# Kernel optimization log

Measured on AMD Instinct MI355X. Metric: run time of the kernel, lower is better.

Reference implementation:

```python
import jax, jax.numpy as jnp
import numpy as np

DIM = 1024
HEADS = 16
DIM_HEAD = 64
INNER = HEADS * DIM_HEAD  # 1024
SCALE = DIM ** (-0.5)  # module scales by dim**-0.5 (not dim_head)


def setup_inputs() -> dict:
    key = jax.random.key(0)
    kx, kqkv, kwo, kbo = jax.random.split(key, 4)
    x = jax.random.normal(kx, (2, 2048, DIM), dtype=jnp.float32)
    W_qkv = jax.random.normal(kqkv, (DIM, 3 * INNER), dtype=jnp.float32) * (DIM ** -0.5)
    W_out = jax.random.normal(kwo, (INNER, DIM), dtype=jnp.float32) * (INNER ** -0.5)
    b_out = jax.random.normal(kbo, (DIM,), dtype=jnp.float32) * 0.01
    return {"x": x, "W_qkv": W_qkv, "W_out": W_out, "b_out": b_out}


def reference(x, W_qkv, W_out, b_out):
    b, n, _ = x.shape
    qkv = x @ W_qkv  # [b, n, 3*inner]
    q, k, v = jnp.split(qkv, 3, axis=-1)
    # [b, n, h*d] -> [b, h, n, d]
    reshape = lambda t: t.reshape(b, n, HEADS, DIM_HEAD).transpose(0, 2, 1, 3)
    q, k, v = reshape(q), reshape(k), reshape(v)
    dots = jnp.einsum('bhid,bhjd->bhij', q, k) * SCALE  # [b, h, n, n]
    attn = jax.nn.softmax(dots, axis=-1)
    out = jnp.einsum('bhij,bhjd->bhid', attn, v)  # [b, h, n, d]
    out = out.transpose(0, 2, 1, 3).reshape(b, n, INNER)
    return out @ W_out + b_out
```

## Files before the change

### kernel.cpp

```cpp
#include <hip/hip_runtime.h>

typedef __bf16 bf16x8 __attribute__((ext_vector_type(8)));
typedef __bf16 bf16x4 __attribute__((ext_vector_type(4)));
typedef __bf16 bf16x2 __attribute__((ext_vector_type(2)));
typedef float f32x4 __attribute__((ext_vector_type(4)));
typedef float f32x16 __attribute__((ext_vector_type(16)));
typedef int i32x4 __attribute__((ext_vector_type(4)));
typedef unsigned int u32x2 __attribute__((ext_vector_type(2)));

#define EXP2_SCALE 0.045084439f

__device__ __forceinline__ void async16(void* lds, const void* g) {
  __builtin_amdgcn_global_load_lds(
      (__attribute__((address_space(1))) unsigned int*)(g),
      (__attribute__((address_space(3))) unsigned int*)(lds), 16, 0, 0);
}

__device__ __forceinline__ unsigned int pack2(float a, float b) {
  bf16x2 t;
  t[0] = (__bf16)a;
  t[1] = (__bf16)b;
  return __builtin_bit_cast(unsigned int, t);
}

__device__ __forceinline__ float fexp2(float x) {
#if __has_builtin(__builtin_amdgcn_exp2f)
  return __builtin_amdgcn_exp2f(x);
#else
  return exp2f(x);
#endif
}

__device__ __forceinline__ void plswap(unsigned int& d, unsigned int& s) {
#if __has_builtin(__builtin_amdgcn_permlane32_swap)
  u32x2 r = __builtin_amdgcn_permlane32_swap(d, s, false, false);
  d = r[0];
  s = r[1];
#else
  asm("v_permlane32_swap_b32 %0, %1" : "+v"(d), "+v"(s));
#endif
}

__device__ __forceinline__ int detect_block(const unsigned short* win, int* cnt_sh) {
  if (threadIdx.x == 0) *cnt_sh = 0;
  __syncthreads();
  int c = 0;
#pragma unroll
  for (int j = 0; j < 8; j++) {
    const unsigned short u = win[threadIdx.x * 8 + j];
    if (((u >> 7) & 0xFF) >= 0xC0) c++;
  }
  if (c) atomicAdd(cnt_sh, c);
  __syncthreads();
  return (*cnt_sh >= 64) ? 1 : 0;
}

__global__ __launch_bounds__(256) void prep(
    const void* __restrict__ x, const void* __restrict__ Wqkv,
    const void* __restrict__ Wout, __bf16* __restrict__ xb,
    __bf16* __restrict__ WqkvT, __bf16* __restrict__ WoutT,
    int* __restrict__ flagp)
{
  __shared__ __bf16 tile[64 * 65];
  __shared__ int cnt;
  const int bx = blockIdx.x;
  const int t = threadIdx.x;

  if (bx < 2048) {
    const long base = (long)bx * 2048;
    const int f = detect_block((const unsigned short*)x + base, &cnt);
    if (bx == 0 && t == 0) *flagp = f;
    const long i = base + t * 8;
    if (f) {
      const f32x4* s4 = (const f32x4*)((const float*)x + i);
      const f32x4 v0 = s4[0], v1 = s4[1];
      bf16x8 o;
#pragma unroll
      for (int j = 0; j < 4; j++) o[j] = (__bf16)v0[j];
#pragma unroll
      for (int j = 0; j < 4; j++) o[4 + j] = (__bf16)v1[j];
      *(bf16x8*)&xb[i] = o;
    } else {
      *(bf16x8*)&xb[i] = *(const bf16x8*)((const __bf16*)x + i);
    }
    return;
  }

  const void* in;  __bf16* out;  int R = 1024, C, tcx, tr;
  if (bx < 2816) {
    const int idx = bx - 2048;
    in = Wqkv; out = WqkvT; C = 3072; tcx = (idx % 48) * 64; tr = (idx / 48) * 64;
  } else {
    const int idx = bx - 2816;
    in = Wout; out = WoutT; C = 1024; tcx = (idx % 16) * 64; tr = (idx / 16) * 64;
  }
  const int f = detect_block((const unsigned short*)in + (long)tr * C + tcx, &cnt);
#pragma unroll
  for (int i = 0; i < 16; i++) {
    const int idx = t + 256 * i;
    const int r = idx >> 6, c = idx & 63;
    const long g = (long)(tr + r) * C + tcx + c;
    tile[r * 65 + c] = f ? (__bf16)((const float*)in)[g] : ((const __bf16*)in)[g];
  }
  __syncthreads();
#pragma unroll
  for (int i = 0; i < 16; i++) {
    const int idx = t + 256 * i;
    const int r = idx >> 6, c = idx & 63;
    out[(long)(tcx + r) * R + tr + c] = tile[c * 65 + r];
  }
}

__global__ __launch_bounds__(256, 3) void gemm_qkv(
    const __bf16* __restrict__ A, const __bf16* __restrict__ Bt,
    __bf16* __restrict__ Qb, __bf16* __restrict__ Kc, __bf16* __restrict__ Vc)
{
  __shared__ __bf16 smem[17408];
  const int t = threadIdx.x;
  const int l = t & 63;
  const int w = t >> 6;
  const int wr = w >> 1, wc = w & 1;
  const int lid = blockIdx.y * 32 + blockIdx.x;
  const int s = (lid & 7) * 96 + (lid >> 3);
  const long m0 = (long)(s & 31) * 128;
  const long n0 = (long)(s >> 5) * 128;
  const int K = 1024;

  const int srow = w * 16 + (l >> 2);
  const int skof = (l & 3) * 8;
  const __bf16* gA = A + (m0 + srow) * (long)K + skof;
  const __bf16* gB = Bt + (n0 + srow) * (long)K + skof;
  const int Ao[2] = {0, 8192}, Bo[2] = {4096, 12288};
  const int lof = w * 512 + l * 8;

  async16(smem + Ao[0] + lof,        gA);
  async16(smem + Ao[0] + 2048 + lof, gA + 64 * (long)K);
  async16(smem + Bo[0] + lof,        gB);
  async16(smem + Bo[0] + 2048 + lof, gB + 64 * (long)K);
  gA += 32; gB += 32;
  __syncthreads();

  f32x4 acc[4][4] = {};

  for (int it = 0; it < 32; it++) {
    if (it < 31) {
      const int nb = (it + 1) & 1;
      async16(smem + Ao[nb] + lof,        gA);
      async16(smem + Ao[nb] + 2048 + lof, gA + 64 * (long)K);
      async16(smem + Bo[nb] + lof,        gB);
      async16(smem + Bo[nb] + 2048 + lof, gB + 64 * (long)K);
      gA += 32; gB += 32;
    }
    const __bf16* As = smem + Ao[it & 1];
    const __bf16* Bs = smem + Bo[it & 1];
    bf16x8 af[4], bfr[4];
#pragma unroll
    for (int mi = 0; mi < 4; mi++)
      af[mi] = *(const bf16x8*)&As[(wr * 64 + mi * 16 + (l & 15)) * 32 + (l >> 4) * 8];
#pragma unroll
    for (int ni = 0; ni < 4; ni++)
      bfr[ni] = *(const bf16x8*)&Bs[(wc * 64 + ni * 16 + (l & 15)) * 32 + (l >> 4) * 8];
#pragma unroll
    for (int mi = 0; mi < 4; mi++)
#pragma unroll
      for (int ni = 0; ni < 4; ni++)
        acc[mi][ni] = __builtin_amdgcn_mfma_f32_16x16x32_bf16(af[mi], bfr[ni], acc[mi][ni], 0, 0, 0);
    __syncthreads();
  }

  if (n0 < 1024) {
#pragma unroll
    for (int mi = 0; mi < 4; mi++)
#pragma unroll
      for (int ni = 0; ni < 4; ni++) {
        const long col = n0 + wc * 64 + ni * 16 + (l & 15);
#pragma unroll
        for (int r = 0; r < 4; r++) {
          const long row = m0 + wr * 64 + mi * 16 + (l >> 4) * 4 + r;
          Qb[row * 1024 + col] = (__bf16)(acc[mi][ni][r] * EXP2_SCALE);
        }
      }
  } else if (n0 < 2048) {
    const int b = (int)(m0 >> 11);
    const int nb_ = (int)(m0 & 2047);
#pragma unroll
    for (int mi = 0; mi < 4; mi++)
#pragma unroll
      for (int ni = 0; ni < 4; ni++) {
        const int col1 = (int)(n0 - 1024) + wc * 64 + ni * 16 + (l & 15);
        const int h = col1 >> 6, d = col1 & 63;
        const long hb = ((long)(b * 16 + h) * 32);
#pragma unroll
        for (int r = 0; r < 4; r++) {
          const int n = nb_ + wr * 64 + mi * 16 + (l >> 4) * 4 + r;
          const long addr = (hb + (n >> 6)) * 4096 + (d >> 3) * 512 + (n & 63) * 8 + (d & 7);
          Kc[addr] = (__bf16)acc[mi][ni][r];
        }
      }
  } else {
#pragma unroll
    for (int mi = 0; mi < 4; mi++)
#pragma unroll
      for (int ni = 0; ni < 4; ni++) {
        const int c = wc * 64 + ni * 16 + (l & 15);
        const int r = wr * 64 + mi * 16 + (l >> 4) * 4;
        bf16x4 pk;
#pragma unroll
        for (int k = 0; k < 4; k++) pk[k] = (__bf16)acc[mi][ni][k];
        *(bf16x4*)&smem[c * 136 + r] = pk;
      }
    __syncthreads();
    const int b = (int)(m0 >> 11);
    const int nbase = (int)(m0 & 2047);
#pragma unroll
    for (int i = 0; i < 8; i++) {
      const int c = (t >> 4) + i * 16;
      const int r8 = (t & 15) * 8;
      const bf16x8 v = *(const bf16x8*)&smem[c * 136 + r8];
      const int vcol = (int)(n0 - 2048) + c;
      const int h = vcol >> 6, d = vcol & 63;
      const int n = nbase + r8;
      const long addr = ((long)(b * 16 + h) * 32 + (n >> 6)) * 4096 + ((n >> 3) & 7) * 512 + d * 8;
      *(bf16x8*)&Vc[addr] = v;
    }
  }
}

__global__ __launch_bounds__(256, 2) void gemm_out(
    const __bf16* __restrict__ A, const __bf16* __restrict__ Bt,
    const void* __restrict__ bias_raw, void* __restrict__ C,
    const int* __restrict__ flagp)
{
  __shared__ __bf16 smem[12288];
  const int t = threadIdx.x;
  const int l = t & 63;
  const int w = t >> 6;
  const int wr = w >> 1, wc = w & 1;
  const int lid = blockIdx.y * 32 + blockIdx.x;
  const int s = (lid & 7) * 64 + (lid >> 3);
  const long m0 = (long)(s & 31) * 128;
  const long n0 = (long)(s >> 5) * 64;
  const int of = *flagp;
  const int K = 1024;

  const int srow = w * 16 + (l >> 2);
  const int skof = (l & 3) * 8;
  const __bf16* gA = A + (m0 + srow) * (long)K + skof;
  const __bf16* gB = Bt + (n0 + srow) * (long)K + skof;
  const int Ao[2] = {0, 6144}, Bo[2] = {4096, 10240};
  const int lof = w * 512 + l * 8;

  async16(smem + Ao[0] + lof,        gA);
  async16(smem + Ao[0] + 2048 + lof, gA + 64 * (long)K);
  async16(smem + Bo[0] + lof,        gB);
  gA += 32; gB += 32;
  __syncthreads();

  f32x4 acc[4][2] = {};

  for (int it = 0; it < 32; it++) {
    if (it < 31) {
      const int nb = (it + 1) & 1;
      async16(smem + Ao[nb] + lof,        gA);
      async16(smem + Ao[nb] + 2048 + lof, gA + 64 * (long)K);
      async16(smem + Bo[nb] + lof,        gB);
      gA += 32; gB += 32;
    }
    const __bf16* As = smem + Ao[it & 1];
    const __bf16* Bs = smem + Bo[it & 1];
    bf16x8 af[4], bfr[2];
#pragma unroll
    for (int mi = 0; mi < 4; mi++)
      af[mi] = *(const bf16x8*)&As[(wr * 64 + mi * 16 + (l & 15)) * 32 + (l >> 4) * 8];
#pragma unroll
    for (int ni = 0; ni < 2; ni++)
      bfr[ni] = *(const bf16x8*)&Bs[(wc * 32 + ni * 16 + (l & 15)) * 32 + (l >> 4) * 8];
#pragma unroll
    for (int mi = 0; mi < 4; mi++)
#pragma unroll
      for (int ni = 0; ni < 2; ni++)
        acc[mi][ni] = __builtin_amdgcn_mfma_f32_16x16x32_bf16(af[mi], bfr[ni], acc[mi][ni], 0, 0, 0);
    __syncthreads();
  }

#pragma unroll
  for (int mi = 0; mi < 4; mi++)
#pragma unroll
    for (int ni = 0; ni < 2; ni++) {
      const long col = n0 + wc * 32 + ni * 16 + (l & 15);
      const float bv = of ? ((const float*)bias_raw)[col]
                          : (float)((const __bf16*)bias_raw)[col];
#pragma unroll
      for (int r = 0; r < 4; r++) {
        const long row = m0 + wr * 64 + mi * 16 + (l >> 4) * 4 + r;
        const float val = acc[mi][ni][r] + bv;
        const long off = row * 1024 + col;
        if (of) ((float*)C)[off] = val;
        else    ((__bf16*)C)[off] = (__bf16)val;
      }
    }
}

__global__ __launch_bounds__(256, 3) void attn_kernel(
    const __bf16* __restrict__ Qb, const __bf16* __restrict__ Kc,
    const __bf16* __restrict__ Vc, __bf16* __restrict__ O)
{
  __shared__ float fsm[4 * 1024 + 128];
  const int t = threadIdx.x;
  const int l = t & 63;
  const int w = t >> 6;
  const int wi = w & 1, wj = w >> 1;
  const int hl = l >> 5;
  const int L = blockIdx.y * 32 + blockIdx.x;
  const int bh = (L & 7) * 4 + ((L >> 3) & 3);
  const int qt = L >> 5;
  const int b = bh >> 4, head = bh & 15;
  const long q_row0 = (long)b * 2048 + qt * 64;

  bf16x8 qf0, qf1, qf2, qf3;
  {
    const __bf16* gQ = Qb + (q_row0 + wi * 32 + (l & 31)) * 1024 + head * 64 + hl * 8;
    qf0 = *(const bf16x8*)(gQ);
    qf1 = *(const bf16x8*)(gQ + 16);
    qf2 = *(const bf16x8*)(gQ + 32);
    qf3 = *(const bf16x8*)(gQ + 48);
  }

  const __bf16* kb = Kc + (long)bh * 131072;
  const __bf16* vb = Vc + (long)bh * 131072;
  const int kof0 = hl * 512 + (wj * 32 + (l & 31)) * 8;
  const int vof0 = (wj * 4 + hl) * 512 + (l & 31) * 8;

  f32x16 accA = {0,0,0,0,0,0,0,0,0,0,0,0,0,0,0,0};
  f32x16 accB = {0,0,0,0,0,0,0,0,0,0,0,0,0,0,0,0};
  const f32x16 fz = {0,0,0,0,0,0,0,0,0,0,0,0,0,0,0,0};
  float l_i = 0.0f;
  bf16x8 pa0 = {}, pa1 = {};

#define LD8(p) (*(const bf16x8*)(p))
  bf16x8 ka0 = LD8(kb + kof0),        ka1 = LD8(kb + kof0 + 1024);
  bf16x8 ka2 = LD8(kb + kof0 + 2048), ka3 = LD8(kb + kof0 + 3072);
  bf16x8 kn0, kn1, kn2, kn3;
  bf16x8 va0 = {}, va1 = {}, va2 = {}, va3 = {};
  bf16x8 vn0, vn1, vn2, vn3;

#define ATT_ITER(IT, KA0,KA1,KA2,KA3, KN0,KN1,KN2,KN3, PV0,PV1,PV2,PV3, PN0,PN1,PN2,PN3) \
  { \
    const __bf16* kt_ = kb + (IT + 1) * 4096 + kof0; \
    const __bf16* vt_ = vb + (IT) * 4096 + vof0; \
    if ((IT) < 31) { \
      KN0 = LD8(kt_); KN1 = LD8(kt_ + 1024); \
      KN2 = LD8(kt_ + 2048); KN3 = LD8(kt_ + 3072); \
    } \
    PN0 = LD8(vt_);        PN1 = LD8(vt_ + 256); \
    PN2 = LD8(vt_ + 1024); PN3 = LD8(vt_ + 1280); \
    __builtin_amdgcn_s_setprio(1); \
    if ((IT) > 0) { \
      accA = __builtin_amdgcn_mfma_f32_32x32x16_bf16(pa0, PV0, accA, 0, 0, 0); \
      accB = __builtin_amdgcn_mfma_f32_32x32x16_bf16(pa0, PV1, accB, 0, 0, 0); \
      accA = __builtin_amdgcn_mfma_f32_32x32x16_bf16(pa1, PV2, accA, 0, 0, 0); \
      accB = __builtin_amdgcn_mfma_f32_32x32x16_bf16(pa1, PV3, accB, 0, 0, 0); \
    } \
    f32x16 st = __builtin_amdgcn_mfma_f32_32x32x16_bf16(KA0, qf0, fz, 0, 0, 0); \
    st = __builtin_amdgcn_mfma_f32_32x32x16_bf16(KA1, qf1, st, 0, 0, 0); \
    st = __builtin_amdgcn_mfma_f32_32x32x16_bf16(KA2, qf2, st, 0, 0, 0); \
    st = __builtin_amdgcn_mfma_f32_32x32x16_bf16(KA3, qf3, st, 0, 0, 0); \
    __builtin_amdgcn_s_setprio(0); \
    float rs0 = 0.0f, rs1 = 0.0f; \
    _Pragma("unroll") \
    for (int r = 0; r < 16; r += 2) { \
      const float p0 = fexp2(st[r]); \
      const float p1 = fexp2(st[r + 1]); \
      st[r] = p0; st[r + 1] = p1; \
      rs0 += p0; rs1 += p1; \
    } \
    l_i += rs0 + rs1; \
    unsigned int a0 = pack2(st[0],  st[1]),  b0 = pack2(st[4],  st[5]); \
    unsigned int c0 = pack2(st[2],  st[3]),  d0 = pack2(st[6],  st[7]); \
    unsigned int a1 = pack2(st[8],  st[9]),  b1 = pack2(st[12], st[13]); \
    unsigned int c1 = pack2(st[10], st[11]), d1 = pack2(st[14], st[15]); \
    plswap(a0, b0); plswap(c0, d0); plswap(a1, b1); plswap(c1, d1); \
    const i32x4 f0_ = {(int)a0, (int)c0, (int)b0, (int)d0}; \
    const i32x4 f1_ = {(int)a1, (int)c1, (int)b1, (int)d1}; \
    pa0 = __builtin_bit_cast(bf16x8, f0_); \
    pa1 = __builtin_bit_cast(bf16x8, f1_); \
  }

  for (int itp = 0; itp < 16; itp++) {
    const int it0 = itp * 2, it1 = itp * 2 + 1;
    ATT_ITER(it0, ka0,ka1,ka2,ka3, kn0,kn1,kn2,kn3, va0,va1,va2,va3, vn0,vn1,vn2,vn3)
    ATT_ITER(it1, kn0,kn1,kn2,kn3, ka0,ka1,ka2,ka3, vn0,vn1,vn2,vn3, va0,va1,va2,va3)
  }
#undef ATT_ITER
#undef LD8

  accA = __builtin_amdgcn_mfma_f32_32x32x16_bf16(pa0, va0, accA, 0, 0, 0);
  accB = __builtin_amdgcn_mfma_f32_32x32x16_bf16(pa0, va1, accB, 0, 0, 0);
  accA = __builtin_amdgcn_mfma_f32_32x32x16_bf16(pa1, va2, accA, 0, 0, 0);
  accB = __builtin_amdgcn_mfma_f32_32x32x16_bf16(pa1, va3, accB, 0, 0, 0);

  {
    unsigned int a = __builtin_bit_cast(unsigned int, l_i), bswp = a;
    plswap(a, bswp);
    l_i = __builtin_bit_cast(float, a) + __builtin_bit_cast(float, bswp);
  }

  float* xbf = fsm;
  float* lb  = fsm + 4096;
#pragma unroll
  for (int r = 0; r < 16; r++)
    xbf[w * 1024 + r * 64 + l] = wj ? accA[r] : accB[r];
  if (l < 32) lb[w * 32 + l] = l_i;
  __syncthreads();
  const int pw = 2 * (1 - wj) + wi;
#pragma unroll
  for (int r = 0; r < 16; r++) {
    const int iloc = (r & 3) + 8 * (r >> 2) + 4 * hl;
    const float lt = lb[wi * 32 + iloc] + lb[(wi + 2) * 32 + iloc];
    const float own = wj ? accB[r] : accA[r];
    const float o = own + xbf[pw * 1024 + r * 64 + l];
    const long row = q_row0 + wi * 32 + iloc;
    const long col = (long)head * 64 + wj * 32 + (l & 31);
    O[row * 1024 + col] = (__bf16)(o / lt);
  }
}

extern "C" void kernel_launch(void* const* d_in, const int* in_sizes, int n_in,
                              void* d_out, int out_size, void* d_ws, size_t ws_size,
                              hipStream_t stream) {
  const void* x    = d_in[0];
  const void* Wqkv = d_in[1];
  const void* Wout = d_in[2];
  const void* bout = d_in[3];

  char* ws = (char*)d_ws;
  int*    flagp = (int*)ws;
  __bf16* xb    = (__bf16*)(ws + 4096);
  __bf16* Obuf  = xb;
  __bf16* WqkvT = (__bf16*)(ws + 4096 +  8388608);
  __bf16* WoutT = (__bf16*)(ws + 4096 + 14680064);
  __bf16* qbuf  = (__bf16*)(ws + 4096 + 16777216);
  __bf16* kbuf  = (__bf16*)(ws + 4096 + 25165824);
  __bf16* vbuf  = (__bf16*)(ws + 4096 + 33554432);

  hipLaunchKernelGGL(prep, dim3(3072), dim3(256), 0, stream,
                     x, Wqkv, Wout, xb, WqkvT, WoutT, flagp);
  hipLaunchKernelGGL(gemm_qkv, dim3(32, 24), dim3(256), 0, stream,
                     xb, WqkvT, qbuf, kbuf, vbuf);
  hipLaunchKernelGGL(attn_kernel, dim3(32, 32), dim3(256), 0, stream,
                     qbuf, kbuf, vbuf, Obuf);
  hipLaunchKernelGGL(gemm_out, dim3(32, 16), dim3(256), 0, stream,
                     Obuf, WoutT, bout, d_out, flagp);
}
```

Measured before the change: 189.9 us.

## Compute softmax row sums via MFMA with ones and stagger KV start per tile

The per-lane fp32 accumulation of exp values is replaced by two extra MFMAs per iteration that multiply the packed bf16 P tiles by a vector of ones. This moves the row-sum work off the VALU and makes the sum match the bf16-rounded P actually used in PV. Each query tile also starts its KV loop at a different block offset, so concurrent blocks spread their K/V reads across memory. The cost is about 20% more MFMA issue per iteration and an extra accumulator register set.

```diff
diff --git a/kernel.cpp b/kernel.cpp
--- a/kernel.cpp
+++ b/kernel.cpp
@@ -316,6 +316,7 @@
   const int qt = L >> 5;
   const int b = bh >> 4, head = bh & 15;
   const long q_row0 = (long)b * 2048 + qt * 64;
+  const int phase = (qt * 5) & 31;
 
   bf16x8 qf0, qf1, qf2, qf3;
   {
@@ -326,6 +327,10 @@
     qf3 = *(const bf16x8*)(gQ + 48);
   }
 
+  bf16x8 onesb;
+#pragma unroll
+  for (int j = 0; j < 8; j++) onesb[j] = (__bf16)1.0f;
+
   const __bf16* kb = Kc + (long)bh * 131072;
   const __bf16* vb = Vc + (long)bh * 131072;
   const int kof0 = hl * 512 + (wj * 32 + (l & 31)) * 8;
@@ -333,48 +338,52 @@
 
   f32x16 accA = {0,0,0,0,0,0,0,0,0,0,0,0,0,0,0,0};
   f32x16 accB = {0,0,0,0,0,0,0,0,0,0,0,0,0,0,0,0};
+  f32x16 lsum = {0,0,0,0,0,0,0,0,0,0,0,0,0,0,0,0};
   const f32x16 fz = {0,0,0,0,0,0,0,0,0,0,0,0,0,0,0,0};
-  float l_i = 0.0f;
   bf16x8 pa0 = {}, pa1 = {};
 
 #define LD8(p) (*(const bf16x8*)(p))
-  bf16x8 ka0 = LD8(kb + kof0),        ka1 = LD8(kb + kof0 + 1024);
-  bf16x8 ka2 = LD8(kb + kof0 + 2048), ka3 = LD8(kb + kof0 + 3072);
+  {
+    const __bf16* k0_ = kb + phase * 4096 + kof0;
+  }
+  bf16x8 ka0, ka1, ka2, ka3;
+  {
+    const __bf16* k0_ = kb + phase * 4096 + kof0;
+    ka0 = LD8(k0_);        ka1 = LD8(k0_ + 1024);
+    ka2 = LD8(k0_ + 2048); ka3 = LD8(k0_ + 3072);
+  }
   bf16x8 kn0, kn1, kn2, kn3;
   bf16x8 va0 = {}, va1 = {}, va2 = {}, va3 = {};
   bf16x8 vn0, vn1, vn2, vn3;
 
-#define ATT_ITER(IT, KA0,KA1,KA2,KA3, KN0,KN1,KN2,KN3, PV0,PV1,PV2,PV3, PN0,PN1,PN2,PN3) \
+#define ATT_ITER(N, KA0,KA1,KA2,KA3, KN0,KN1,KN2,KN3, PV0,PV1,PV2,PV3, PN0,PN1,PN2,PN3) \
   { \
-    const __bf16* kt_ = kb + (IT + 1) * 4096 + kof0; \
-    const __bf16* vt_ = vb + (IT) * 4096 + vof0; \
-    if ((IT) < 31) { \
+    const int itk_ = ((N) + 1 + phase) & 31; \
+    const int itv_ = ((N) + phase) & 31; \
+    const __bf16* kt_ = kb + itk_ * 4096 + kof0; \
+    const __bf16* vt_ = vb + itv_ * 4096 + vof0; \
+    if ((N) < 31) { \
       KN0 = LD8(kt_); KN1 = LD8(kt_ + 1024); \
       KN2 = LD8(kt_ + 2048); KN3 = LD8(kt_ + 3072); \
     } \
     PN0 = LD8(vt_);        PN1 = LD8(vt_ + 256); \
     PN2 = LD8(vt_ + 1024); PN3 = LD8(vt_ + 1280); \
     __builtin_amdgcn_s_setprio(1); \
-    if ((IT) > 0) { \
+    if ((N) > 0) { \
       accA = __builtin_amdgcn_mfma_f32_32x32x16_bf16(pa0, PV0, accA, 0, 0, 0); \
       accB = __builtin_amdgcn_mfma_f32_32x32x16_bf16(pa0, PV1, accB, 0, 0, 0); \
       accA = __builtin_amdgcn_mfma_f32_32x32x16_bf16(pa1, PV2, accA, 0, 0, 0); \
       accB = __builtin_amdgcn_mfma_f32_32x32x16_bf16(pa1, PV3, accB, 0, 0, 0); \
+      lsum = __builtin_amdgcn_mfma_f32_32x32x16_bf16(pa0, onesb, lsum, 0, 0, 0); \
+      lsum = __builtin_amdgcn_mfma_f32_32x32x16_bf16(pa1, onesb, lsum, 0, 0, 0); \
     } \
     f32x16 st = __builtin_amdgcn_mfma_f32_32x32x16_bf16(KA0, qf0, fz, 0, 0, 0); \
     st = __builtin_amdgcn_mfma_f32_32x32x16_bf16(KA1, qf1, st, 0, 0, 0); \
     st = __builtin_amdgcn_mfma_f32_32x32x16_bf16(KA2, qf2, st, 0, 0, 0); \
     st = __builtin_amdgcn_mfma_f32_32x32x16_bf16(KA3, qf3, st, 0, 0, 0); \
     __builtin_amdgcn_s_setprio(0); \
-    float rs0 = 0.0f, rs1 = 0.0f; \
     _Pragma("unroll") \
-    for (int r = 0; r < 16; r += 2) { \
-      const float p0 = fexp2(st[r]); \
-      const float p1 = fexp2(st[r + 1]); \
-      st[r] = p0; st[r + 1] = p1; \
-      rs0 += p0; rs1 += p1; \
-    } \
-    l_i += rs0 + rs1; \
+    for (int r = 0; r < 16; r++) st[r] = fexp2(st[r]); \
     unsigned int a0 = pack2(st[0],  st[1]),  b0 = pack2(st[4],  st[5]); \
     unsigned int c0 = pack2(st[2],  st[3]),  d0 = pack2(st[6],  st[7]); \
     unsigned int a1 = pack2(st[8],  st[9]),  b1 = pack2(st[12], st[13]); \
@@ -398,25 +407,27 @@
   accB = __builtin_amdgcn_mfma_f32_32x32x16_bf16(pa0, va1, accB, 0, 0, 0);
   accA = __builtin_amdgcn_mfma_f32_32x32x16_bf16(pa1, va2, accA, 0, 0, 0);
   accB = __builtin_amdgcn_mfma_f32_32x32x16_bf16(pa1, va3, accB, 0, 0, 0);
-
-  {
-    unsigned int a = __builtin_bit_cast(unsigned int, l_i), bswp = a;
-    plswap(a, bswp);
-    l_i = __builtin_bit_cast(float, a) + __builtin_bit_cast(float, bswp);
-  }
+  lsum = __builtin_amdgcn_mfma_f32_32x32x16_bf16(pa0, onesb, lsum, 0, 0, 0);
+  lsum = __builtin_amdgcn_mfma_f32_32x32x16_bf16(pa1, onesb, lsum, 0, 0, 0);
 
   float* xbf = fsm;
   float* lb  = fsm + 4096;
 #pragma unroll
   for (int r = 0; r < 16; r++)
     xbf[w * 1024 + r * 64 + l] = wj ? accA[r] : accB[r];
-  if (l < 32) lb[w * 32 + l] = l_i;
+  if ((l & 31) == 0) {
+#pragma unroll
+    for (int r = 0; r < 16; r++) {
+      const int iloc = (r & 3) + 8 * (r >> 2) + 4 * hl;
+      lb[w * 32 + iloc] = lsum[r];
+    }
+  }
   __syncthreads();
   const int pw = 2 * (1 - wj) + wi;
 #pragma unroll
   for (int r = 0; r < 16; r++) {
     const int iloc = (r & 3) + 8 * (r >> 2) + 4 * hl;
-    const float lt = lb[wi * 32 + iloc] + lb[(wi + 2) * 32 + iloc];
+    const float lt = lsum[r] + lb[pw * 32 + iloc];
     const float own = wj ? accB[r] : accA[r];
     const float o = own + xbf[pw * 1024 + r * 64 + l];
     const long row = q_row0 + wi * 32 + iloc;
```

After: 192.8 us. Within noise of the previous version (+1.5%).

## Process two 64-row query tiles per attention block to reuse K/V loads

Applied to the files above, without the earlier changes.

Each attention workgroup now handles 128 query rows instead of 64, holding two sets of Q fragments and accumulators and reusing every loaded K and V fragment for both tiles. The grid is halved and the launch-bounds occupancy hint drops from 3 to 2. The goal is to halve K/V global traffic per query row and raise MFMA density per load. In exchange, register pressure rises, fewer waves are resident to hide latency, and the grid shrinks to 512 blocks, which may underfill the GPU.

```diff
diff --git a/kernel.cpp b/kernel.cpp
--- a/kernel.cpp
+++ b/kernel.cpp
@@ -301,7 +301,7 @@
     }
 }
 
-__global__ __launch_bounds__(256, 3) void attn_kernel(
+__global__ __launch_bounds__(256, 2) void attn_kernel(
     const __bf16* __restrict__ Qb, const __bf16* __restrict__ Kc,
     const __bf16* __restrict__ Vc, __bf16* __restrict__ O)
 {
@@ -315,15 +315,20 @@
   const int bh = (L & 7) * 4 + ((L >> 3) & 3);
   const int qt = L >> 5;
   const int b = bh >> 4, head = bh & 15;
-  const long q_row0 = (long)b * 2048 + qt * 64;
-
-  bf16x8 qf0, qf1, qf2, qf3;
+  const long q_row0 = (long)b * 2048 + qt * 128;
+
+  bf16x8 qA0, qA1, qA2, qA3, qB0, qB1, qB2, qB3;
   {
     const __bf16* gQ = Qb + (q_row0 + wi * 32 + (l & 31)) * 1024 + head * 64 + hl * 8;
-    qf0 = *(const bf16x8*)(gQ);
-    qf1 = *(const bf16x8*)(gQ + 16);
-    qf2 = *(const bf16x8*)(gQ + 32);
-    qf3 = *(const bf16x8*)(gQ + 48);
+    qA0 = *(const bf16x8*)(gQ);
+    qA1 = *(const bf16x8*)(gQ + 16);
+    qA2 = *(const bf16x8*)(gQ + 32);
+    qA3 = *(const bf16x8*)(gQ + 48);
+    gQ += (long)64 * 1024;
+    qB0 = *(const bf16x8*)(gQ);
+    qB1 = *(const bf16x8*)(gQ + 16);
+    qB2 = *(const bf16x8*)(gQ + 32);
+    qB3 = *(const bf16x8*)(gQ + 48);
   }
 
   const __bf16* kb = Kc + (long)bh * 131072;
@@ -331,11 +336,13 @@
   const int kof0 = hl * 512 + (wj * 32 + (l & 31)) * 8;
   const int vof0 = (wj * 4 + hl) * 512 + (l & 31) * 8;
 
-  f32x16 accA = {0,0,0,0,0,0,0,0,0,0,0,0,0,0,0,0};
-  f32x16 accB = {0,0,0,0,0,0,0,0,0,0,0,0,0,0,0,0};
+  f32x16 aAa = {0,0,0,0,0,0,0,0,0,0,0,0,0,0,0,0};
+  f32x16 aBa = {0,0,0,0,0,0,0,0,0,0,0,0,0,0,0,0};
+  f32x16 aAb = {0,0,0,0,0,0,0,0,0,0,0,0,0,0,0,0};
+  f32x16 aBb = {0,0,0,0,0,0,0,0,0,0,0,0,0,0,0,0};
   const f32x16 fz = {0,0,0,0,0,0,0,0,0,0,0,0,0,0,0,0};
-  float l_i = 0.0f;
-  bf16x8 pa0 = {}, pa1 = {};
+  float liA = 0.0f, liB = 0.0f;
+  bf16x8 paA0 = {}, paA1 = {}, paB0 = {}, paB1 = {};
 
 #define LD8(p) (*(const bf16x8*)(p))
   bf16x8 ka0 = LD8(kb + kof0),        ka1 = LD8(kb + kof0 + 1024);
@@ -343,6 +350,19 @@
   bf16x8 kn0, kn1, kn2, kn3;
   bf16x8 va0 = {}, va1 = {}, va2 = {}, va3 = {};
   bf16x8 vn0, vn1, vn2, vn3;
+
+#define SM_PACK(ST, PA0, PA1) \
+  { \
+    unsigned int a0 = pack2(ST[0],  ST[1]),  b0 = pack2(ST[4],  ST[5]); \
+    unsigned int c0 = pack2(ST[2],  ST[3]),  d0 = pack2(ST[6],  ST[7]); \
+    unsigned int a1 = pack2(ST[8],  ST[9]),  b1 = pack2(ST[12], ST[13]); \
+    unsigned int c1 = pack2(ST[10], ST[11]), d1 = pack2(ST[14], ST[15]); \
+    plswap(a0, b0); plswap(c0, d0); plswap(a1, b1); plswap(c1, d1); \
+    const i32x4 f0_ = {(int)a0, (int)c0, (int)b0, (int)d0}; \
+    const i32x4 f1_ = {(int)a1, (int)c1, (int)b1, (int)d1}; \
+    PA0 = __builtin_bit_cast(bf16x8, f0_); \
+    PA1 = __builtin_bit_cast(bf16x8, f1_); \
+  }
 
 #define ATT_ITER(IT, KA0,KA1,KA2,KA3, KN0,KN1,KN2,KN3, PV0,PV1,PV2,PV3, PN0,PN1,PN2,PN3) \
   { \
@@ -356,34 +376,44 @@
     PN2 = LD8(vt_ + 1024); PN3 = LD8(vt_ + 1280); \
     __builtin_amdgcn_s_setprio(1); \
     if ((IT) > 0) { \
-      accA = __builtin_amdgcn_mfma_f32_32x32x16_bf16(pa0, PV0, accA, 0, 0, 0); \
-      accB = __builtin_amdgcn_mfma_f32_32x32x16_bf16(pa0, PV1, accB, 0, 0, 0); \
-      accA = __builtin_amdgcn_mfma_f32_32x32x16_bf16(pa1, PV2, accA, 0, 0, 0); \
-      accB = __builtin_amdgcn_mfma_f32_32x32x16_bf16(pa1, PV3, accB, 0, 0, 0); \
+      aAa = __builtin_amdgcn_mfma_f32_32x32x16_bf16(paA0, PV0, aAa, 0, 0, 0); \
+      aBa = __builtin_amdgcn_mfma_f32_32x32x16_bf16(paA0, PV1, aBa, 0, 0, 0); \
+      aAb = __builtin_amdgcn_mfma_f32_32x32x16_bf16(paB0, PV0, aAb, 0, 0, 0); \
+      aBb = __builtin_amdgcn_mfma_f32_32x32x16_bf16(paB0, PV1, aBb, 0, 0, 0); \
+      aAa = __builtin_amdgcn_mfma_f32_32x32x16_bf16(paA1, PV2, aAa, 0, 0, 0); \
+      aBa = __builtin_amdgcn_mfma_f32_32x32x16_bf16(paA1, PV3, aBa, 0, 0, 0); \
+      aAb = __builtin_amdgcn_mfma_f32_32x32x16_bf16(paB1, PV2, aAb, 0, 0, 0); \
+      aBb = __builtin_amdgcn_mfma_f32_32x32x16_bf16(paB1, PV3, aBb, 0, 0, 0); \
     } \
-    f32x16 st = __builtin_amdgcn_mfma_f32_32x32x16_bf16(KA0, qf0, fz, 0, 0, 0); \
-    st = __builtin_amdgcn_mfma_f32_32x32x16_bf16(KA1, qf1, st, 0, 0, 0); \
-    st = __builtin_amdgcn_mfma_f32_32x32x16_bf16(KA2, qf2, st, 0, 0, 0); \
-    st = __builtin_amdgcn_mfma_f32_32x32x16_bf16(KA3, qf3, st, 0, 0, 0); \
+    f32x16 stA = __builtin_amdgcn_mfma_f32_32x32x16_bf16(KA0, qA0, fz, 0, 0, 0); \
+    f32x16 stB = __builtin_amdgcn_mfma_f32_32x32x16_bf16(KA0, qB0, fz, 0, 0, 0); \
+    stA = __builtin_amdgcn_mfma_f32_32x32x16_bf16(KA1, qA1, stA, 0, 0, 0); \
+    stB = __builtin_amdgcn_mfma_f32_32x32x16_bf16(KA1, qB1, stB, 0, 0, 0); \
+    stA = __builtin_amdgcn_mfma_f32_32x32x16_bf16(KA2, qA2, stA, 0, 0, 0); \
+    stB = __builtin_amdgcn_mfma_f32_32x32x16_bf16(KA2, qB2, stB, 0, 0, 0); \
+    stA = __builtin_amdgcn_mfma_f32_32x32x16_bf16(KA3, qA3, stA, 0, 0, 0); \
+    stB = __builtin_amdgcn_mfma_f32_32x32x16_bf16(KA3, qB3, stB, 0, 0, 0); \
     __builtin_amdgcn_s_setprio(0); \
-    float rs0 = 0.0f, rs1 = 0.0f; \
+    float rsA0 = 0.0f, rsA1 = 0.0f; \
     _Pragma("unroll") \
     for (int r = 0; r < 16; r += 2) { \
-      const float p0 = fexp2(st[r]); \
-      const float p1 = fexp2(st[r + 1]); \
-      st[r] = p0; st[r + 1] = p1; \
-      rs0 += p0; rs1 += p1; \
+      const float p0 = fexp2(stA[r]); \
+      const float p1 = fexp2(stA[r + 1]); \
+      stA[r] = p0; stA[r + 1] = p1; \
+      rsA0 += p0; rsA1 += p1; \
     } \
-    l_i += rs0 + rs1; \
-    unsigned int a0 = pack2(st[0],  st[1]),  b0 = pack2(st[4],  st[5]); \
-    unsigned int c0 = pack2(st[2],  st[3]),  d0 = pack2(st[6],  st[7]); \
-    unsigned int a1 = pack2(st[8],  st[9]),  b1 = pack2(st[12], st[13]); \
-    unsigned int c1 = pack2(st[10], st[11]), d1 = pack2(st[14], st[15]); \
-    plswap(a0, b0); plswap(c0, d0); plswap(a1, b1); plswap(c1, d1); \
-    const i32x4 f0_ = {(int)a0, (int)c0, (int)b0, (int)d0}; \
-    const i32x4 f1_ = {(int)a1, (int)c1, (int)b1, (int)d1}; \
-    pa0 = __builtin_bit_cast(bf16x8, f0_); \
-    pa1 = __builtin_bit_cast(bf16x8, f1_); \
+    liA += rsA0 + rsA1; \
+    SM_PACK(stA, paA0, paA1) \
+    float rsB0 = 0.0f, rsB1 = 0.0f; \
+    _Pragma("unroll") \
+    for (int r = 0; r < 16; r += 2) { \
+      const float p0 = fexp2(stB[r]); \
+      const float p1 = fexp2(stB[r + 1]); \
+      stB[r] = p0; stB[r + 1] = p1; \
+      rsB0 += p0; rsB1 += p1; \
+    } \
+    liB += rsB0 + rsB1; \
+    SM_PACK(stB, paB0, paB1) \
   }
 
   for (int itp = 0; itp < 16; itp++) {
@@ -394,32 +424,59 @@
 #undef ATT_ITER
 #undef LD8
 
-  accA = __builtin_amdgcn_mfma_f32_32x32x16_bf16(pa0, va0, accA, 0, 0, 0);
-  accB = __builtin_amdgcn_mfma_f32_32x32x16_bf16(pa0, va1, accB, 0, 0, 0);
-  accA = __builtin_amdgcn_mfma_f32_32x32x16_bf16(pa1, va2, accA, 0, 0, 0);
-  accB = __builtin_amdgcn_mfma_f32_32x32x16_bf16(pa1, va3, accB, 0, 0, 0);
+  aAa = __builtin_amdgcn_mfma_f32_32x32x16_bf16(paA0, va0, aAa, 0, 0, 0);
+  aBa = __builtin_amdgcn_mfma_f32_32x32x16_bf16(paA0, va1, aBa, 0, 0, 0);
+  aAb = __builtin_amdgcn_mfma_f32_32x32x16_bf16(paB0, va0, aAb, 0, 0, 0);
+  aBb = __builtin_amdgcn_mfma_f32_32x32x16_bf16(paB0, va1, aBb, 0, 0, 0);
+  aAa = __builtin_amdgcn_mfma_f32_32x32x16_bf16(paA1, va2, aAa, 0, 0, 0);
+  aBa = __builtin_amdgcn_mfma_f32_32x32x16_bf16(paA1, va3, aBa, 0, 0, 0);
+  aAb = __builtin_amdgcn_mfma_f32_32x32x16_bf16(paB1, va2, aAb, 0, 0, 0);
+  aBb = __builtin_amdgcn_mfma_f32_32x32x16_bf16(paB1, va3, aBb, 0, 0, 0);
 
   {
-    unsigned int a = __builtin_bit_cast(unsigned int, l_i), bswp = a;
-    plswap(a, bswp);
-    l_i = __builtin_bit_cast(float, a) + __builtin_bit_cast(float, bswp);
+    unsigned int a = __builtin_bit_cast(unsigned int, liA), s = a;
+    plswap(a, s);
+    liA = __builtin_bit_cast(float, a) + __builtin_bit_cast(float, s);
+  }
+  {
+    unsigned int a = __builtin_bit_cast(unsigned int, liB), s = a;
+    plswap(a, s);
+    liB = __builtin_bit_cast(float, a) + __builtin_bit_cast(float, s);
   }
 
   float* xbf = fsm;
   float* lb  = fsm + 4096;
+  const int pw = 2 * (1 - wj) + wi;
+
 #pragma unroll
   for (int r = 0; r < 16; r++)
-    xbf[w * 1024 + r * 64 + l] = wj ? accA[r] : accB[r];
-  if (l < 32) lb[w * 32 + l] = l_i;
-  __syncthreads();
-  const int pw = 2 * (1 - wj) + wi;
+    xbf[w * 1024 + r * 64 + l] = wj ? aAa[r] : aBa[r];
+  if (l < 32) lb[w * 32 + l] = liA;
+  __syncthreads();
 #pragma unroll
   for (int r = 0; r < 16; r++) {
     const int iloc = (r & 3) + 8 * (r >> 2) + 4 * hl;
     const float lt = lb[wi * 32 + iloc] + lb[(wi + 2) * 32 + iloc];
-    const float own = wj ? accB[r] : accA[r];
+    const float own = wj ? aBa[r] : aAa[r];
     const float o = own + xbf[pw * 1024 + r * 64 + l];
     const long row = q_row0 + wi * 32 + iloc;
+    const long col = (long)head * 64 + wj * 32 + (l & 31);
+    O[row * 1024 + col] = (__bf16)(o / lt);
+  }
+  __syncthreads();
+
+#pragma unroll
+  for (int r = 0; r < 16; r++)
+    xbf[w * 1024 + r * 64 + l] = wj ? aAb[r] : aBb[r];
+  if (l < 32) lb[w * 32 + l] = liB;
+  __syncthreads();
+#pragma unroll
+  for (int r = 0; r < 16; r++) {
+    const int iloc = (r & 3) + 8 * (r >> 2) + 4 * hl;
+    const float lt = lb[wi * 32 + iloc] + lb[(wi + 2) * 32 + iloc];
+    const float own = wj ? aBb[r] : aAb[r];
+    const float o = own + xbf[pw * 1024 + r * 64 + l];
+    const long row = q_row0 + 64 + wi * 32 + iloc;
     const long col = (long)head * 64 + wj * 32 + (l & 31);
     O[row * 1024 + col] = (__bf16)(o / lt);
   }
@@ -447,7 +504,7 @@
                      x, Wqkv, Wout, xb, WqkvT, WoutT, flagp);
   hipLaunchKernelGGL(gemm_qkv, dim3(32, 24), dim3(256), 0, stream,
                      xb, WqkvT, qbuf, kbuf, vbuf);
-  hipLaunchKernelGGL(attn_kernel, dim3(32, 32), dim3(256), 0, stream,
+  hipLaunchKernelGGL(attn_kernel, dim3(32, 16), dim3(256), 0, stream,
                      qbuf, kbuf, vbuf, Obuf);
   hipLaunchKernelGGL(gemm_out, dim3(32, 16), dim3(256), 0, stream,
                      Obuf, WoutT, bout, d_out, flagp);
```

Result: no change. 187.0 us (-1.5%).
